# Kernel optimization log

Hardware: AMD Instinct MI355X
Metric: run time of the kernel (lower is better)

The kernel has to match this reference:

```python
import jax, jax.numpy as jnp
from jax import lax
import numpy as np

ALPHA = 0.5
MAX_ITERS = 40
TOL = 1e-6
BITS = 8


def fake_quant_sym(w, bits=BITS):
    # symmetric per-tensor fake quantisation
    qmax = float(2 ** (bits - 1) - 1)
    scale = jnp.max(jnp.abs(w)) / qmax
    return jnp.round(w / scale) * scale


def fb_solve(Wq, Uq, bq, x, alpha=ALPHA, max_iters=MAX_ITERS, tol=TOL):
    # forward-backward splitting fixed-point solve: z = relu((1-a)z + a(Wz + Ux^T + b))
    n = Wq.shape[0]
    B = x.shape[0]
    Ux = Uq @ x.T + bq[:, None]  # (n, B), constant across iterations

    def cond(carry):
        z, res, it = carry
        return jnp.logical_and(it < max_iters, res >= tol)

    def body(carry):
        z, _, it = carry
        u = (1.0 - alpha) * z + alpha * (Wq @ z + Ux)
        z_next = jax.nn.relu(u)  # relu_prox
        res = jnp.linalg.norm(z_next - z) / (jnp.linalg.norm(z) + 1e-12)
        return z_next, res, it + 1

    z0 = jnp.zeros((n, B), dtype=x.dtype)
    z, _, _ = lax.while_loop(cond, body, (z0, jnp.array(jnp.inf, dtype=x.dtype), 0))
    u_star = (1.0 - alpha) * z + alpha * (Wq @ z + Ux)
    mask = (u_star > 0).astype(x.dtype)  # relu Jacobian mask D*
    return z, mask


def setup_inputs() -> dict:
    key = jax.random.key(0)
    k0, k1, k2, k3, k4 = jax.random.split(key, 5)
    n, d, B, C = 512, 784, 128, 10
    # scale W so ||W||_2 < 1 (monotone operator condition m > 0)
    W = 0.3 * jax.random.normal(k0, (n, n), dtype=jnp.float32) / jnp.sqrt(n)
    U = jax.random.normal(k1, (n, d), dtype=jnp.float32) / jnp.sqrt(d)
    b = 0.01 * jax.random.normal(k2, (n,), dtype=jnp.float32)
    x = jax.random.normal(k3, (B, d), dtype=jnp.float32)
    Wc = jax.random.normal(k4, (C, n), dtype=jnp.float32) / jnp.sqrt(n)
    bc = jnp.zeros((C,), dtype=jnp.float32)
    return {"W": W, "U": U, "b": b, "x": x, "Wc": Wc, "bc": bc}


def reference(W, U, b, x, Wc, bc):
    # post-training fake quantisation of W, U, b (done once at init in torch)
    Wq = fake_quant_sym(W)
    Uq = fake_quant_sym(U)
    bq = fake_quant_sym(b)
    z_star, _ = fb_solve(Wq, Uq, bq, x)  # (n, B)
    logits = z_star.T @ Wc.T + bc  # classifier on z*^T
    return logits
```

## Files before the change

### kernel.cpp

```cpp
#include <hip/hip_runtime.h>
#include <hip/hip_bf16.h>


#define N_DIM 512
#define D_DIM 784
#define B_DIM 128
#define C_DIM 10
#define QMAX 127.0f
#define N_ITERS 40
#define HILO_START 28
#define ZPITCH 528
#define MT 2
#define XPITCH 800
#define QUPITCH 808

typedef int    i32x4  __attribute__((ext_vector_type(4)));
typedef float  f32x4  __attribute__((ext_vector_type(4)));
typedef __bf16 bf16x8 __attribute__((ext_vector_type(8)));
typedef short  s16x2  __attribute__((ext_vector_type(2)));

#define WSF_PW  0
#define WSF_PU  64
#define WSF_SB  128
#define WSF_BQ  192
#define WSF_XH  704
#define WSF_XL  (WSF_XH + 51200)
#define WSF_QP8 (WSF_XL + 51200)
#define WSF_UXT (WSF_QP8 + 65536)

__device__ __forceinline__ float pscale64(const float* __restrict__ p) {
    float m = 0.0f;
#pragma unroll 16
    for (int i = 0; i < 64; ++i) m = fmaxf(m, p[i]);
    return m * (1.0f / QMAX);
}

__device__ __forceinline__ void pack_hl(const int vq[4], unsigned int& h, unsigned int& l) {
    int pk01, pk23;
#if __has_builtin(__builtin_amdgcn_cvt_pk_i16)
    union { s16x2 v; int i; } u0, u1;
    u0.v = __builtin_amdgcn_cvt_pk_i16(vq[0], vq[1]);
    u1.v = __builtin_amdgcn_cvt_pk_i16(vq[2], vq[3]);
    pk01 = u0.i; pk23 = u1.i;
#else
    asm("v_cvt_pk_i16_i32 %0, %1, %2" : "=v"(pk01) : "v"(vq[0]), "v"(vq[1]));
    asm("v_cvt_pk_i16_i32 %0, %1, %2" : "=v"(pk23) : "v"(vq[2]), "v"(vq[3]));
#endif
    h = __builtin_amdgcn_perm((unsigned int)pk23, (unsigned int)pk01, 0x07050301u);
    l = __builtin_amdgcn_perm((unsigned int)pk23, (unsigned int)pk01, 0x06040200u) ^ 0x80808080u;
}

__global__ __launch_bounds__(256) void scales_kernel(const float* __restrict__ W,
                                                     const float* __restrict__ U,
                                                     const float* __restrict__ b,
                                                     const float* __restrict__ x,
                                                     float* __restrict__ ws) {
    __shared__ float ls[4];
    __shared__ float sbS;
    const int t = threadIdx.x, wave = t >> 6, lane = t & 63;
    const int bid = blockIdx.x;
    if (bid < 128) {
        const float4* src; int n4, rb;
        if (bid < 64) { src = (const float4*)W; n4 = N_DIM * N_DIM / 4; rb = bid; }
        else          { src = (const float4*)U; n4 = N_DIM * D_DIM / 4; rb = bid - 64; }
        float mv = 0.0f;
        for (int i = rb * 256 + t; i < n4; i += 64 * 256) {
            float4 v = src[i];
            mv = fmaxf(mv, fmaxf(fmaxf(fabsf(v.x), fabsf(v.y)), fmaxf(fabsf(v.z), fabsf(v.w))));
        }
#pragma unroll
        for (int s = 1; s < 64; s <<= 1) mv = fmaxf(mv, __shfl_xor(mv, s));
        if (lane == 0) ls[wave] = mv;
        __syncthreads();
        if (t == 0) ws[bid] = fmaxf(fmaxf(ls[0], ls[1]), fmaxf(ls[2], ls[3]));
    } else if (bid == 128) {
        float4 v = {0.0f, 0.0f, 0.0f, 0.0f};
        if (t < N_DIM / 4) v = ((const float4*)b)[t];
        float mv = fmaxf(fmaxf(fabsf(v.x), fabsf(v.y)), fmaxf(fabsf(v.z), fabsf(v.w)));
#pragma unroll
        for (int s = 1; s < 64; s <<= 1) mv = fmaxf(mv, __shfl_xor(mv, s));
        if (lane == 0) ls[wave] = mv;
        __syncthreads();
        if (t == 0) {
            float m = fmaxf(fmaxf(ls[0], ls[1]), fmaxf(ls[2], ls[3]));
            float sb = m * (1.0f / QMAX);
            ws[WSF_SB] = sb;
            sbS = sb;
        }
        __syncthreads();
        if (t < N_DIM / 4) {
            const float sb = sbS;
            float4 o;
            o.x = rintf(v.x / sb) * sb;
            o.y = rintf(v.y / sb) * sb;
            o.z = rintf(v.z / sb) * sb;
            o.w = rintf(v.w / sb) * sb;
            ((float4*)(ws + WSF_BQ))[t] = o;
        }
    } else {
        __bf16* xh = (__bf16*)(ws + WSF_XH);
        __bf16* xl = (__bf16*)(ws + WSF_XL);
        const int xb = bid - 129;
        for (int i = xb * 256 + t; i < 128 * 196; i += 64 * 256) {
            int r = i / 196, kf = i - r * 196;
            float4 v = *(const float4*)&x[r * D_DIM + (kf << 2)];
            union { __bf16 e[4]; ushort4 u; } hh, ll;
            __bf16 h0 = (__bf16)v.x, h1 = (__bf16)v.y, h2 = (__bf16)v.z, h3 = (__bf16)v.w;
            hh.e[0] = h0; hh.e[1] = h1; hh.e[2] = h2; hh.e[3] = h3;
            ll.e[0] = (__bf16)(v.x - (float)h0);
            ll.e[1] = (__bf16)(v.y - (float)h1);
            ll.e[2] = (__bf16)(v.z - (float)h2);
            ll.e[3] = (__bf16)(v.w - (float)h3);
            *(ushort4*)&xh[r * XPITCH + (kf << 2)] = hh.u;
            *(ushort4*)&xl[r * XPITCH + (kf << 2)] = ll.u;
        }
        if (xb == 0) {
            int r = t >> 1, c = D_DIM + (t & 1) * 8;
            ushort4 z = {0, 0, 0, 0};
            *(ushort4*)&xh[r * XPITCH + c] = z; *(ushort4*)&xh[r * XPITCH + c + 4] = z;
            *(ushort4*)&xl[r * XPITCH + c] = z; *(ushort4*)&xl[r * XPITCH + c + 4] = z;
        }
    }
}

__global__ __launch_bounds__(256) void prep_kernel(const float* __restrict__ W,
                                                   const float* __restrict__ U,
                                                   float* __restrict__ ws,
                                                   signed char* __restrict__ Qp8) {
    __shared__ __bf16 quS[16][QUPITCH];
    const int t = threadIdx.x;
    const int wave = t >> 6, lane = t & 63;
    const int bid = blockIdx.x;
    if (bid < 256) {
        const float s = pscale64(ws + WSF_PW);
        const float inv = 1.0f / s;
        int idx = bid * 256 + t;
        float4 w = ((const float4*)W)[idx];
        int k = (idx << 2) & (N_DIM - 1);
        int r = (idx << 2) >> 9;
        char4 c;
        c.x = (signed char)(int)rintf(w.x * inv);
        c.y = (signed char)(int)rintf(w.y * inv);
        c.z = (signed char)(int)rintf(w.z * inv);
        c.w = (signed char)(int)rintf(w.w * inv);
        int kc = k >> 6, q = (k >> 4) & 3, jj = k & 15;
        *(char4*)&Qp8[((kc << 9) + r) * 64 + q * 16 + jj] = c;
    } else {
        const float sU = pscale64(ws + WSF_PU);
        const float invU = 1.0f / sU;
        const int i0 = (bid - 256) * 16;
        for (int i = t; i < 16 * 196; i += 256) {
            int r = i / 196, kf = i - r * 196;
            float4 v = *(const float4*)&U[(i0 + r) * D_DIM + (kf << 2)];
            union { __bf16 e[4]; ushort4 u; } q;
            q.e[0] = (__bf16)rintf(v.x * invU);
            q.e[1] = (__bf16)rintf(v.y * invU);
            q.e[2] = (__bf16)rintf(v.z * invU);
            q.e[3] = (__bf16)rintf(v.w * invU);
            *(ushort4*)&quS[r][kf << 2] = q.u;
        }
        { int r = t >> 4, k = D_DIM + (t & 15); quS[r][k] = (__bf16)0.0f; }
        __syncthreads();
        const int m = lane & 15, quad = lane >> 4;
        const __bf16* xh = (const __bf16*)(ws + WSF_XH);
        const __bf16* xl = (const __bf16*)(ws + WSF_XL);
        const float* bq = ws + WSF_BQ;
        float* UxT = ws + WSF_UXT;
        const int row0 = i0 + (quad << 2);
        const f32x4 bqv = *(const f32x4*)&bq[row0];
        for (int cg = wave; cg < 8; cg += 4) {
            const __bf16* xhr = &xh[(cg * 16 + m) * XPITCH];
            const __bf16* xlr = &xl[(cg * 16 + m) * XPITCH];
            f32x4 acc = {};
#pragma unroll 5
            for (int kc = 0; kc < 25; ++kc) {
                bf16x8 au = *(const bf16x8*)&quS[m][kc * 32 + (quad << 3)];
                bf16x8 bh = *(const bf16x8*)&xhr[kc * 32 + (quad << 3)];
                bf16x8 bl = *(const bf16x8*)&xlr[kc * 32 + (quad << 3)];
                acc = __builtin_amdgcn_mfma_f32_16x16x32_bf16(au, bh, acc, 0, 0, 0);
                acc = __builtin_amdgcn_mfma_f32_16x16x32_bf16(au, bl, acc, 0, 0, 0);
            }
            f32x4 o;
#pragma unroll
            for (int r = 0; r < 4; ++r) o[r] = sU * acc[r] + bqv[r];
            *(f32x4*)&UxT[(cg * 16 + m) * N_DIM + row0] = o;
        }
    }
}

__global__ __launch_bounds__(1024, 1) void solve_kernel(const signed char* __restrict__ Qp8,
                                                        const float* __restrict__ UxT,
                                                        const float* __restrict__ wsf,
                                                        const float* __restrict__ Wc,
                                                        const float* __restrict__ bc,
                                                        float* __restrict__ out) {
    __shared__ signed char zh[2][16][ZPITCH];
    __shared__ signed char zl[2][16][ZPITCH];
    __shared__ float red[16][16][C_DIM];
    const int t = threadIdx.x;
    const int wave = t >> 6;
    const int lane = t & 63;
    const int m = lane & 15;
    const int quad = lane >> 4;
    const int c0 = blockIdx.x * 16;
    const float sW = pscale64(wsf + WSF_PW);
    const float c1 = sW * (1.0f / 2048.0f);
    const float hc_hi = c1 * 128.0f;
    const float g_hi = sW * 128.0f;
    const float g_lo = sW * 0.5f;
    const int rowbase = wave * 32;

    i32x4 A[MT][8];
#pragma unroll
    for (int ti = 0; ti < MT; ++ti)
#pragma unroll
        for (int kc = 0; kc < 8; ++kc)
            A[ti][kc] = *(const i32x4*)&Qp8[((kc << 9) + rowbase + ti * 16 + m) * 64 + (quad << 4)];

    const i32x4 onesb = {0x01010101, 0x01010101, 0x01010101, 0x01010101};
    i32x4 rs[MT];
#pragma unroll
    for (int ti = 0; ti < MT; ++ti) {
        i32x4 a = {};
#pragma unroll
        for (int kc = 0; kc < 8; ++kc)
            a = __builtin_amdgcn_mfma_i32_16x16x64_i8(A[ti][kc], onesb, a, 0, 0, 0);
        rs[ti] = a;
    }

    float Z[MT][4];
    float UX2[MT][4];
#pragma unroll
    for (int ti = 0; ti < MT; ++ti) {
        const int row0 = rowbase + ti * 16 + (quad << 2);
        const f32x4 v4 = *(const f32x4*)&UxT[(c0 + m) * N_DIM + row0];
        int vq[4];
#pragma unroll
        for (int r = 0; r < 4; ++r) {
            const float v = v4[r];
            const float uxh = 0.5f * (v + hc_hi * (float)rs[ti][r]);
            UX2[ti][r] = uxh * 2048.0f;
            const float z1 = fmaxf(0.5f * v, 0.0f);
            const float Z1 = z1 * 2048.0f;
            Z[ti][r] = Z1;
            vq[r] = (int)rintf(Z1);
        }
        unsigned int h, l;
        pack_hl(vq, h, l);
        *(unsigned int*)&zh[0][m][row0] = h;
        *(unsigned int*)&zl[0][m][row0] = l;
    }

#pragma unroll
    for (int ti = 0; ti < MT; ++ti)
#pragma unroll
        for (int kc = 0; kc < 8; ++kc)
            asm volatile("" : "+v"(A[ti][kc]));
    __syncthreads();

    int cur = 0;
    for (int it = 1; it < N_ITERS; ++it) {
        const bool lo = (it >= HILO_START);
        const bool wlo = (it >= HILO_START - 1);
        i32x4 acch[MT] = {};
        i32x4 accl[MT] = {};
        if (lo) {
#pragma unroll
            for (int kc = 0; kc < 8; ++kc) {
                i32x4 bh = *(const i32x4*)&zh[cur][m][(kc << 6) + (quad << 4)];
                i32x4 bl = *(const i32x4*)&zl[cur][m][(kc << 6) + (quad << 4)];
#pragma unroll
                for (int ti = 0; ti < MT; ++ti) {
                    acch[ti] = __builtin_amdgcn_mfma_i32_16x16x64_i8(A[ti][kc], bh, acch[ti], 0, 0, 0);
                    accl[ti] = __builtin_amdgcn_mfma_i32_16x16x64_i8(A[ti][kc], bl, accl[ti], 0, 0, 0);
                }
            }
        } else {
#pragma unroll
            for (int kc = 0; kc < 8; ++kc) {
                i32x4 bh = *(const i32x4*)&zh[cur][m][(kc << 6) + (quad << 4)];
#pragma unroll
                for (int ti = 0; ti < MT; ++ti)
                    acch[ti] = __builtin_amdgcn_mfma_i32_16x16x64_i8(A[ti][kc], bh, acch[ti], 0, 0, 0);
            }
        }
        const int nxt = cur ^ 1;
#pragma unroll
        for (int ti = 0; ti < MT; ++ti) {
            const int row0 = rowbase + ti * 16 + (quad << 2);
            int vq[4];
#pragma unroll
            for (int r = 0; r < 4; ++r) {
                float base = fmaf(0.5f, Z[ti][r], UX2[ti][r]);
                float u = lo ? fmaf(g_hi, (float)acch[ti][r], fmaf(g_lo, (float)accl[ti][r], base))
                             : fmaf(g_hi, (float)acch[ti][r], base);
                float Zn = fmaxf(u, 0.0f);
                Z[ti][r] = Zn;
                vq[r] = (int)rintf(Zn);
            }
            unsigned int h, l;
            pack_hl(vq, h, l);
            *(unsigned int*)&zh[nxt][m][row0] = h;
            if (wlo) *(unsigned int*)&zl[nxt][m][row0] = l;
        }
        __syncthreads();
        cur = nxt;
    }

    {
        float p[C_DIM];
#pragma unroll
        for (int cl = 0; cl < C_DIM; ++cl) p[cl] = 0.0f;
#pragma unroll
        for (int ti = 0; ti < MT; ++ti) {
            const int row0 = rowbase + ti * 16 + (quad << 2);
#pragma unroll
            for (int r = 0; r < 4; ++r) {
                float zv = Z[ti][r] * (1.0f / 2048.0f);
#pragma unroll
                for (int cl = 0; cl < C_DIM; ++cl)
                    p[cl] += zv * Wc[cl * N_DIM + row0 + r];
            }
        }
#pragma unroll
        for (int cl = 0; cl < C_DIM; ++cl) {
            p[cl] += __shfl_xor(p[cl], 16);
            p[cl] += __shfl_xor(p[cl], 32);
        }
        if (lane < 16) {
#pragma unroll
            for (int cl = 0; cl < C_DIM; ++cl) red[wave][lane][cl] = p[cl];
        }
        __syncthreads();
        for (int s = 8; s > 0; s >>= 1) {
            if (wave < s && lane < 16) {
#pragma unroll
                for (int cl = 0; cl < C_DIM; ++cl)
                    red[wave][lane][cl] += red[wave + s][lane][cl];
            }
            __syncthreads();
        }
        if (t < 16 * C_DIM) {
            int col = t & 15;
            int cl  = t >> 4;
            out[(c0 + col) * C_DIM + cl] = red[0][col][cl] + bc[cl];
        }
    }
}

extern "C" void kernel_launch(void* const* d_in, const int* in_sizes, int n_in,
                              void* d_out, int out_size, void* d_ws, size_t ws_size,
                              hipStream_t stream) {
    const float* W  = (const float*)d_in[0];
    const float* U  = (const float*)d_in[1];
    const float* b  = (const float*)d_in[2];
    const float* x  = (const float*)d_in[3];
    const float* Wc = (const float*)d_in[4];
    const float* bc = (const float*)d_in[5];
    float* out = (float*)d_out;

    float* ws = (float*)d_ws;
    signed char* Qp8 = (signed char*)(ws + WSF_QP8);
    float* UxT = ws + WSF_UXT;

    scales_kernel<<<193, 256, 0, stream>>>(W, U, b, x, ws);
    prep_kernel<<<288, 256, 0, stream>>>(W, U, ws, Qp8);
    solve_kernel<<<8, 1024, 0, stream>>>(Qp8, UxT, ws, Wc, bc, out);
}
```

Baseline: 142.4 us.

## Fuse weight quantisation and Ux projection into the solve kernel, drop prep kernel

Removes the separate prep kernel and its workspace round-trips. Each solve block now quantises its own slice of W straight into int8 MFMA registers, splits its 16 batch columns of x into bf16 hi/lo in shared memory, and computes the quantised-U projection plus quantised bias in-register. This saves a kernel launch and the global writes and reads of the packed W and UxT. In exchange, each of the 8 blocks re-reads and re-quantises all of U and W from fp32, so redundant work and global traffic grow and run inside a grid with very few blocks.

```diff
diff --git a/kernel.cpp b/kernel.cpp
--- a/kernel.cpp
+++ b/kernel.cpp
@@ -11,8 +11,7 @@
 #define HILO_START 28
 #define ZPITCH 528
 #define MT 2
-#define XPITCH 800
-#define QUPITCH 808
+#define XPITCH 808
 
 typedef int    i32x4  __attribute__((ext_vector_type(4)));
 typedef float  f32x4  __attribute__((ext_vector_type(4)));
@@ -22,17 +21,26 @@
 #define WSF_PW  0
 #define WSF_PU  64
 #define WSF_SB  128
-#define WSF_BQ  192
-#define WSF_XH  704
-#define WSF_XL  (WSF_XH + 51200)
-#define WSF_QP8 (WSF_XL + 51200)
-#define WSF_UXT (WSF_QP8 + 65536)
 
 __device__ __forceinline__ float pscale64(const float* __restrict__ p) {
     float m = 0.0f;
 #pragma unroll 16
     for (int i = 0; i < 64; ++i) m = fmaxf(m, p[i]);
     return m * (1.0f / QMAX);
+}
+
+__device__ __forceinline__ int pack_lo4(int q0, int q1, int q2, int q3) {
+    int pk01, pk23;
+#if __has_builtin(__builtin_amdgcn_cvt_pk_i16)
+    union { s16x2 v; int i; } u0, u1;
+    u0.v = __builtin_amdgcn_cvt_pk_i16(q0, q1);
+    u1.v = __builtin_amdgcn_cvt_pk_i16(q2, q3);
+    pk01 = u0.i; pk23 = u1.i;
+#else
+    asm("v_cvt_pk_i16_i32 %0, %1, %2" : "=v"(pk01) : "v"(q0), "v"(q1));
+    asm("v_cvt_pk_i16_i32 %0, %1, %2" : "=v"(pk23) : "v"(q2), "v"(q3));
+#endif
+    return (int)__builtin_amdgcn_perm((unsigned int)pk23, (unsigned int)pk01, 0x06040200u);
 }
 
 __device__ __forceinline__ void pack_hl(const int vq[4], unsigned int& h, unsigned int& l) {
@@ -53,10 +61,8 @@
 __global__ __launch_bounds__(256) void scales_kernel(const float* __restrict__ W,
                                                      const float* __restrict__ U,
                                                      const float* __restrict__ b,
-                                                     const float* __restrict__ x,
                                                      float* __restrict__ ws) {
     __shared__ float ls[4];
-    __shared__ float sbS;
     const int t = threadIdx.x, wave = t >> 6, lane = t & 63;
     const int bid = blockIdx.x;
     if (bid < 128) {
@@ -73,7 +79,7 @@
         if (lane == 0) ls[wave] = mv;
         __syncthreads();
         if (t == 0) ws[bid] = fmaxf(fmaxf(ls[0], ls[1]), fmaxf(ls[2], ls[3]));
-    } else if (bid == 128) {
+    } else {
         float4 v = {0.0f, 0.0f, 0.0f, 0.0f};
         if (t < N_DIM / 4) v = ((const float4*)b)[t];
         float mv = fmaxf(fmaxf(fabsf(v.x), fabsf(v.y)), fmaxf(fabsf(v.z), fabsf(v.w)));
@@ -81,121 +87,22 @@
         for (int s = 1; s < 64; s <<= 1) mv = fmaxf(mv, __shfl_xor(mv, s));
         if (lane == 0) ls[wave] = mv;
         __syncthreads();
-        if (t == 0) {
-            float m = fmaxf(fmaxf(ls[0], ls[1]), fmaxf(ls[2], ls[3]));
-            float sb = m * (1.0f / QMAX);
-            ws[WSF_SB] = sb;
-            sbS = sb;
-        }
-        __syncthreads();
-        if (t < N_DIM / 4) {
-            const float sb = sbS;
-            float4 o;
-            o.x = rintf(v.x / sb) * sb;
-            o.y = rintf(v.y / sb) * sb;
-            o.z = rintf(v.z / sb) * sb;
-            o.w = rintf(v.w / sb) * sb;
-            ((float4*)(ws + WSF_BQ))[t] = o;
-        }
-    } else {
-        __bf16* xh = (__bf16*)(ws + WSF_XH);
-        __bf16* xl = (__bf16*)(ws + WSF_XL);
-        const int xb = bid - 129;
-        for (int i = xb * 256 + t; i < 128 * 196; i += 64 * 256) {
-            int r = i / 196, kf = i - r * 196;
-            float4 v = *(const float4*)&x[r * D_DIM + (kf << 2)];
-            union { __bf16 e[4]; ushort4 u; } hh, ll;
-            __bf16 h0 = (__bf16)v.x, h1 = (__bf16)v.y, h2 = (__bf16)v.z, h3 = (__bf16)v.w;
-            hh.e[0] = h0; hh.e[1] = h1; hh.e[2] = h2; hh.e[3] = h3;
-            ll.e[0] = (__bf16)(v.x - (float)h0);
-            ll.e[1] = (__bf16)(v.y - (float)h1);
-            ll.e[2] = (__bf16)(v.z - (float)h2);
-            ll.e[3] = (__bf16)(v.w - (float)h3);
-            *(ushort4*)&xh[r * XPITCH + (kf << 2)] = hh.u;
-            *(ushort4*)&xl[r * XPITCH + (kf << 2)] = ll.u;
-        }
-        if (xb == 0) {
-            int r = t >> 1, c = D_DIM + (t & 1) * 8;
-            ushort4 z = {0, 0, 0, 0};
-            *(ushort4*)&xh[r * XPITCH + c] = z; *(ushort4*)&xh[r * XPITCH + c + 4] = z;
-            *(ushort4*)&xl[r * XPITCH + c] = z; *(ushort4*)&xl[r * XPITCH + c + 4] = z;
-        }
-    }
-}
-
-__global__ __launch_bounds__(256) void prep_kernel(const float* __restrict__ W,
-                                                   const float* __restrict__ U,
-                                                   float* __restrict__ ws,
-                                                   signed char* __restrict__ Qp8) {
-    __shared__ __bf16 quS[16][QUPITCH];
-    const int t = threadIdx.x;
-    const int wave = t >> 6, lane = t & 63;
-    const int bid = blockIdx.x;
-    if (bid < 256) {
-        const float s = pscale64(ws + WSF_PW);
-        const float inv = 1.0f / s;
-        int idx = bid * 256 + t;
-        float4 w = ((const float4*)W)[idx];
-        int k = (idx << 2) & (N_DIM - 1);
-        int r = (idx << 2) >> 9;
-        char4 c;
-        c.x = (signed char)(int)rintf(w.x * inv);
-        c.y = (signed char)(int)rintf(w.y * inv);
-        c.z = (signed char)(int)rintf(w.z * inv);
-        c.w = (signed char)(int)rintf(w.w * inv);
-        int kc = k >> 6, q = (k >> 4) & 3, jj = k & 15;
-        *(char4*)&Qp8[((kc << 9) + r) * 64 + q * 16 + jj] = c;
-    } else {
-        const float sU = pscale64(ws + WSF_PU);
-        const float invU = 1.0f / sU;
-        const int i0 = (bid - 256) * 16;
-        for (int i = t; i < 16 * 196; i += 256) {
-            int r = i / 196, kf = i - r * 196;
-            float4 v = *(const float4*)&U[(i0 + r) * D_DIM + (kf << 2)];
-            union { __bf16 e[4]; ushort4 u; } q;
-            q.e[0] = (__bf16)rintf(v.x * invU);
-            q.e[1] = (__bf16)rintf(v.y * invU);
-            q.e[2] = (__bf16)rintf(v.z * invU);
-            q.e[3] = (__bf16)rintf(v.w * invU);
-            *(ushort4*)&quS[r][kf << 2] = q.u;
-        }
-        { int r = t >> 4, k = D_DIM + (t & 15); quS[r][k] = (__bf16)0.0f; }
-        __syncthreads();
-        const int m = lane & 15, quad = lane >> 4;
-        const __bf16* xh = (const __bf16*)(ws + WSF_XH);
-        const __bf16* xl = (const __bf16*)(ws + WSF_XL);
-        const float* bq = ws + WSF_BQ;
-        float* UxT = ws + WSF_UXT;
-        const int row0 = i0 + (quad << 2);
-        const f32x4 bqv = *(const f32x4*)&bq[row0];
-        for (int cg = wave; cg < 8; cg += 4) {
-            const __bf16* xhr = &xh[(cg * 16 + m) * XPITCH];
-            const __bf16* xlr = &xl[(cg * 16 + m) * XPITCH];
-            f32x4 acc = {};
-#pragma unroll 5
-            for (int kc = 0; kc < 25; ++kc) {
-                bf16x8 au = *(const bf16x8*)&quS[m][kc * 32 + (quad << 3)];
-                bf16x8 bh = *(const bf16x8*)&xhr[kc * 32 + (quad << 3)];
-                bf16x8 bl = *(const bf16x8*)&xlr[kc * 32 + (quad << 3)];
-                acc = __builtin_amdgcn_mfma_f32_16x16x32_bf16(au, bh, acc, 0, 0, 0);
-                acc = __builtin_amdgcn_mfma_f32_16x16x32_bf16(au, bl, acc, 0, 0, 0);
-            }
-            f32x4 o;
-#pragma unroll
-            for (int r = 0; r < 4; ++r) o[r] = sU * acc[r] + bqv[r];
-            *(f32x4*)&UxT[(cg * 16 + m) * N_DIM + row0] = o;
-        }
-    }
-}
-
-__global__ __launch_bounds__(1024, 1) void solve_kernel(const signed char* __restrict__ Qp8,
-                                                        const float* __restrict__ UxT,
+        if (t == 0) ws[WSF_SB] = fmaxf(fmaxf(ls[0], ls[1]), fmaxf(ls[2], ls[3]));
+    }
+}
+
+__global__ __launch_bounds__(1024, 1) void solve_kernel(const float* __restrict__ W,
+                                                        const float* __restrict__ U,
+                                                        const float* __restrict__ b,
+                                                        const float* __restrict__ x,
                                                         const float* __restrict__ wsf,
                                                         const float* __restrict__ Wc,
                                                         const float* __restrict__ bc,
                                                         float* __restrict__ out) {
     __shared__ signed char zh[2][16][ZPITCH];
     __shared__ signed char zl[2][16][ZPITCH];
+    __shared__ __bf16 xhS[16][XPITCH];
+    __shared__ __bf16 xlS[16][XPITCH];
     __shared__ float red[16][16][C_DIM];
     const int t = threadIdx.x;
     const int wave = t >> 6;
@@ -204,18 +111,52 @@
     const int quad = lane >> 4;
     const int c0 = blockIdx.x * 16;
     const float sW = pscale64(wsf + WSF_PW);
+    const float sU = pscale64(wsf + WSF_PU);
+    const float invW = 1.0f / sW;
+    const float invU = 1.0f / sU;
+    const float sb = wsf[WSF_SB] * (1.0f / QMAX);
     const float c1 = sW * (1.0f / 2048.0f);
     const float hc_hi = c1 * 128.0f;
     const float g_hi = sW * 128.0f;
     const float g_lo = sW * 0.5f;
     const int rowbase = wave * 32;
 
+    for (int i = t; i < 16 * 196; i += 1024) {
+        int r = i / 196, kf = i - r * 196;
+        float4 v = *(const float4*)&x[(c0 + r) * D_DIM + (kf << 2)];
+        union { __bf16 e[4]; ushort4 u; } hh, ll;
+        __bf16 h0 = (__bf16)v.x, h1 = (__bf16)v.y, h2 = (__bf16)v.z, h3 = (__bf16)v.w;
+        hh.e[0] = h0; hh.e[1] = h1; hh.e[2] = h2; hh.e[3] = h3;
+        ll.e[0] = (__bf16)(v.x - (float)h0);
+        ll.e[1] = (__bf16)(v.y - (float)h1);
+        ll.e[2] = (__bf16)(v.z - (float)h2);
+        ll.e[3] = (__bf16)(v.w - (float)h3);
+        *(ushort4*)&xhS[r][kf << 2] = hh.u;
+        *(ushort4*)&xlS[r][kf << 2] = ll.u;
+    }
+    if (t < 64) {
+        int r = t >> 2, cpad = D_DIM + (t & 3) * 4;
+        ushort4 z4 = {0, 0, 0, 0};
+        *(ushort4*)&xhS[r][cpad] = z4;
+        *(ushort4*)&xlS[r][cpad] = z4;
+    }
+
     i32x4 A[MT][8];
 #pragma unroll
     for (int ti = 0; ti < MT; ++ti)
 #pragma unroll
-        for (int kc = 0; kc < 8; ++kc)
-            A[ti][kc] = *(const i32x4*)&Qp8[((kc << 9) + rowbase + ti * 16 + m) * 64 + (quad << 4)];
+        for (int kc = 0; kc < 8; ++kc) {
+            const float4* wr = (const float4*)&W[(rowbase + ti * 16 + m) * N_DIM
+                                                 + (kc << 6) + (quad << 4)];
+            i32x4 a;
+#pragma unroll
+            for (int j = 0; j < 4; ++j) {
+                float4 w = wr[j];
+                a[j] = pack_lo4((int)rintf(w.x * invW), (int)rintf(w.y * invW),
+                                (int)rintf(w.z * invW), (int)rintf(w.w * invW));
+            }
+            A[ti][kc] = a;
+        }
 
     const i32x4 onesb = {0x01010101, 0x01010101, 0x01010101, 0x01010101};
     i32x4 rs[MT];
@@ -228,16 +169,40 @@
         rs[ti] = a;
     }
 
+    __syncthreads();
+
+    f32x4 uacc[MT] = {};
+#pragma unroll 5
+    for (int kc = 0; kc < 25; ++kc) {
+        const int kb = kc * 32 + (quad << 3);
+        bf16x8 bh = *(const bf16x8*)&xhS[m][kb];
+        bf16x8 bl = *(const bf16x8*)&xlS[m][kb];
+        const int k0 = (kb <= D_DIM - 8) ? kb : (D_DIM - 8);
+#pragma unroll
+        for (int ti = 0; ti < MT; ++ti) {
+            const float4* ur = (const float4*)&U[(rowbase + ti * 16 + m) * D_DIM + k0];
+            float4 u0 = ur[0], u1 = ur[1];
+            bf16x8 au;
+            au[0] = (__bf16)rintf(u0.x * invU); au[1] = (__bf16)rintf(u0.y * invU);
+            au[2] = (__bf16)rintf(u0.z * invU); au[3] = (__bf16)rintf(u0.w * invU);
+            au[4] = (__bf16)rintf(u1.x * invU); au[5] = (__bf16)rintf(u1.y * invU);
+            au[6] = (__bf16)rintf(u1.z * invU); au[7] = (__bf16)rintf(u1.w * invU);
+            uacc[ti] = __builtin_amdgcn_mfma_f32_16x16x32_bf16(au, bh, uacc[ti], 0, 0, 0);
+            uacc[ti] = __builtin_amdgcn_mfma_f32_16x16x32_bf16(au, bl, uacc[ti], 0, 0, 0);
+        }
+    }
+
     float Z[MT][4];
     float UX2[MT][4];
 #pragma unroll
     for (int ti = 0; ti < MT; ++ti) {
         const int row0 = rowbase + ti * 16 + (quad << 2);
-        const f32x4 v4 = *(const f32x4*)&UxT[(c0 + m) * N_DIM + row0];
+        const f32x4 bv = *(const f32x4*)&b[row0];
         int vq[4];
 #pragma unroll
         for (int r = 0; r < 4; ++r) {
-            const float v = v4[r];
+            const float bqv = rintf(bv[r] / sb) * sb;
+            const float v = sU * uacc[ti][r] + bqv;
             const float uxh = 0.5f * (v + hc_hi * (float)rs[ti][r]);
             UX2[ti][r] = uxh * 2048.0f;
             const float z1 = fmaxf(0.5f * v, 0.0f);
@@ -358,12 +323,8 @@
     const float* Wc = (const float*)d_in[4];
     const float* bc = (const float*)d_in[5];
     float* out = (float*)d_out;
-
     float* ws = (float*)d_ws;
-    signed char* Qp8 = (signed char*)(ws + WSF_QP8);
-    float* UxT = ws + WSF_UXT;
-
-    scales_kernel<<<193, 256, 0, stream>>>(W, U, b, x, ws);
-    prep_kernel<<<288, 256, 0, stream>>>(W, U, ws, Qp8);
-    solve_kernel<<<8, 1024, 0, stream>>>(Qp8, UxT, ws, Wc, bc, out);
-}
+
+    scales_kernel<<<129, 256, 0, stream>>>(W, U, b, ws);
+    solve_kernel<<<8, 1024, 0, stream>>>(W, U, b, x, ws, Wc, bc, out);
+}
```

Measured after the change: 178.9 us. 1.26x slower.

## Fuse prep and solve kernels with atomic-counter producer/consumer sync

Applied to the files above, without the earlier changes.

Merges the quantisation/Ux prep kernel and the fixed-point solve kernel into one launch of 104 blocks of 1024 threads. 96 producer blocks quantise W and compute UxT, then each increments a global counter with release semantics. The 8 solver blocks spin on the counter until all producers finish, then run the solve. This removes a kernel launch boundary and its tail. The risks are deadlock if the solver blocks are scheduled before the producers can run, and less parallelism in prep because it now uses fewer, larger blocks.

```diff
diff --git a/kernel.cpp b/kernel.cpp
--- a/kernel.cpp
+++ b/kernel.cpp
@@ -22,11 +22,14 @@
 #define WSF_PW  0
 #define WSF_PU  64
 #define WSF_SB  128
+#define WSF_CNT 160
 #define WSF_BQ  192
 #define WSF_XH  704
 #define WSF_XL  (WSF_XH + 51200)
 #define WSF_QP8 (WSF_XL + 51200)
 #define WSF_UXT (WSF_QP8 + 65536)
+
+#define N_PRODUCERS 96
 
 __device__ __forceinline__ float pscale64(const float* __restrict__ p) {
     float m = 0.0f;
@@ -74,6 +77,7 @@
         __syncthreads();
         if (t == 0) ws[bid] = fmaxf(fmaxf(ls[0], ls[1]), fmaxf(ls[2], ls[3]));
     } else if (bid == 128) {
+        if (t == 0) ((int*)ws)[WSF_CNT] = 0;
         float4 v = {0.0f, 0.0f, 0.0f, 0.0f};
         if (t < N_DIM / 4) v = ((const float4*)b)[t];
         float mv = fmaxf(fmaxf(fabsf(v.x), fabsf(v.y)), fmaxf(fabsf(v.z), fabsf(v.w)));
@@ -123,18 +127,23 @@
     }
 }
 
-__global__ __launch_bounds__(256) void prep_kernel(const float* __restrict__ W,
-                                                   const float* __restrict__ U,
-                                                   float* __restrict__ ws,
-                                                   signed char* __restrict__ Qp8) {
-    __shared__ __bf16 quS[16][QUPITCH];
+__global__ __launch_bounds__(1024, 1) void fused_kernel(const float* __restrict__ W,
+                                                        const float* __restrict__ U,
+                                                        float* __restrict__ ws,
+                                                        const float* __restrict__ Wc,
+                                                        const float* __restrict__ bc,
+                                                        float* __restrict__ out) {
+    __shared__ __align__(16) char LDS[44032];
     const int t = threadIdx.x;
     const int wave = t >> 6, lane = t & 63;
     const int bid = blockIdx.x;
-    if (bid < 256) {
+    signed char* Qp8 = (signed char*)(ws + WSF_QP8);
+    int* cnt = (int*)ws + WSF_CNT;
+
+    if (bid < 64) {
         const float s = pscale64(ws + WSF_PW);
         const float inv = 1.0f / s;
-        int idx = bid * 256 + t;
+        int idx = bid * 1024 + t;
         float4 w = ((const float4*)W)[idx];
         int k = (idx << 2) & (N_DIM - 1);
         int r = (idx << 2) >> 9;
@@ -145,11 +154,16 @@
         c.w = (signed char)(int)rintf(w.w * inv);
         int kc = k >> 6, q = (k >> 4) & 3, jj = k & 15;
         *(char4*)&Qp8[((kc << 9) + r) * 64 + q * 16 + jj] = c;
-    } else {
+        __syncthreads();
+        if (t == 0) __hip_atomic_fetch_add(cnt, 1, __ATOMIC_RELEASE, __HIP_MEMORY_SCOPE_AGENT);
+        return;
+    }
+    if (bid < 96) {
+        __bf16 (*quS)[QUPITCH] = (__bf16 (*)[QUPITCH])LDS;
         const float sU = pscale64(ws + WSF_PU);
         const float invU = 1.0f / sU;
-        const int i0 = (bid - 256) * 16;
-        for (int i = t; i < 16 * 196; i += 256) {
+        const int i0 = (bid - 64) * 16;
+        for (int i = t; i < 16 * 196; i += 1024) {
             int r = i / 196, kf = i - r * 196;
             float4 v = *(const float4*)&U[(i0 + r) * D_DIM + (kf << 2)];
             union { __bf16 e[4]; ushort4 u; } q;
@@ -159,16 +173,17 @@
             q.e[3] = (__bf16)rintf(v.w * invU);
             *(ushort4*)&quS[r][kf << 2] = q.u;
         }
-        { int r = t >> 4, k = D_DIM + (t & 15); quS[r][k] = (__bf16)0.0f; }
-        __syncthreads();
-        const int m = lane & 15, quad = lane >> 4;
-        const __bf16* xh = (const __bf16*)(ws + WSF_XH);
-        const __bf16* xl = (const __bf16*)(ws + WSF_XL);
-        const float* bq = ws + WSF_BQ;
-        float* UxT = ws + WSF_UXT;
-        const int row0 = i0 + (quad << 2);
-        const f32x4 bqv = *(const f32x4*)&bq[row0];
-        for (int cg = wave; cg < 8; cg += 4) {
+        if (t < 256) { int r = t >> 4, k = D_DIM + (t & 15); quS[r][k] = (__bf16)0.0f; }
+        __syncthreads();
+        if (wave < 8) {
+            const int m = lane & 15, quad = lane >> 4;
+            const __bf16* xh = (const __bf16*)(ws + WSF_XH);
+            const __bf16* xl = (const __bf16*)(ws + WSF_XL);
+            const float* bq = ws + WSF_BQ;
+            float* UxT = ws + WSF_UXT;
+            const int row0 = i0 + (quad << 2);
+            const f32x4 bqv = *(const f32x4*)&bq[row0];
+            const int cg = wave;
             const __bf16* xhr = &xh[(cg * 16 + m) * XPITCH];
             const __bf16* xlr = &xl[(cg * 16 + m) * XPITCH];
             f32x4 acc = {};
@@ -185,25 +200,26 @@
             for (int r = 0; r < 4; ++r) o[r] = sU * acc[r] + bqv[r];
             *(f32x4*)&UxT[(cg * 16 + m) * N_DIM + row0] = o;
         }
-    }
-}
-
-__global__ __launch_bounds__(1024, 1) void solve_kernel(const signed char* __restrict__ Qp8,
-                                                        const float* __restrict__ UxT,
-                                                        const float* __restrict__ wsf,
-                                                        const float* __restrict__ Wc,
-                                                        const float* __restrict__ bc,
-                                                        float* __restrict__ out) {
-    __shared__ signed char zh[2][16][ZPITCH];
-    __shared__ signed char zl[2][16][ZPITCH];
-    __shared__ float red[16][16][C_DIM];
-    const int t = threadIdx.x;
-    const int wave = t >> 6;
-    const int lane = t & 63;
+        __syncthreads();
+        if (t == 0) __hip_atomic_fetch_add(cnt, 1, __ATOMIC_RELEASE, __HIP_MEMORY_SCOPE_AGENT);
+        return;
+    }
+
+    if (t == 0) {
+        while (__hip_atomic_load(cnt, __ATOMIC_RELAXED, __HIP_MEMORY_SCOPE_AGENT) < N_PRODUCERS)
+            __builtin_amdgcn_s_sleep(8);
+    }
+    __syncthreads();
+    (void)__hip_atomic_load(cnt, __ATOMIC_ACQUIRE, __HIP_MEMORY_SCOPE_AGENT);
+
+    signed char (*zh)[16][ZPITCH] = (signed char (*)[16][ZPITCH])(LDS);
+    signed char (*zl)[16][ZPITCH] = (signed char (*)[16][ZPITCH])(LDS + 16896);
+    float (*red)[16][C_DIM]       = (float (*)[16][C_DIM])(LDS + 33792);
+    const float* UxT = ws + WSF_UXT;
     const int m = lane & 15;
     const int quad = lane >> 4;
-    const int c0 = blockIdx.x * 16;
-    const float sW = pscale64(wsf + WSF_PW);
+    const int c0 = (bid - 96) * 16;
+    const float sW = pscale64(ws + WSF_PW);
     const float c1 = sW * (1.0f / 2048.0f);
     const float hc_hi = c1 * 128.0f;
     const float g_hi = sW * 128.0f;
@@ -358,12 +374,8 @@
     const float* Wc = (const float*)d_in[4];
     const float* bc = (const float*)d_in[5];
     float* out = (float*)d_out;
-
     float* ws = (float*)d_ws;
-    signed char* Qp8 = (signed char*)(ws + WSF_QP8);
-    float* UxT = ws + WSF_UXT;
 
     scales_kernel<<<193, 256, 0, stream>>>(W, U, b, x, ws);
-    prep_kernel<<<288, 256, 0, stream>>>(W, U, ws, Qp8);
-    solve_kernel<<<8, 1024, 0, stream>>>(Qp8, UxT, ws, Wc, bc, out);
-}
+    fused_kernel<<<104, 1024, 0, stream>>>(W, U, ws, Wc, bc, out);
+}
```

New measurement: 141.4 us. About the same (-0.7%).
